# Optimization experiments

Hardware: AMD Instinct MI355X
Metric: run time of the kernel (lower is better)

## Reference

```python
import jax, jax.numpy as jnp
import numpy as np

T, Z, D_DIM = 8, 2048, 1024
N_EXP, P_SLOT, H = 64, 32, 1024
LN_EPS = 1e-5


def setup_inputs() -> dict:
    key = jax.random.key(0)
    k = jax.random.split(key, 5)
    s = 0.02
    return {
        "x": jax.random.normal(k[0], (T, Z, D_DIM), dtype=jnp.float32),
        "phi_w": jax.random.normal(k[1], (N_EXP * P_SLOT, D_DIM), dtype=jnp.float32) * s,
        "phi_b": jax.random.normal(k[2], (N_EXP * P_SLOT,), dtype=jnp.float32) * s,
        "expert_w": jax.random.normal(k[3], (N_EXP, D_DIM, H), dtype=jnp.float32) * s,
        "expert_b": jax.random.normal(k[4], (N_EXP, H), dtype=jnp.float32) * s,
    }


def reference(x, phi_w, phi_b, expert_w, expert_b):
    t, z, d = x.shape
    n = expert_w.shape[0]
    p = phi_w.shape[0] // n
    # routing logits: [t, z, n, p]
    logits = (jnp.einsum('tzd,ed->tze', x, phi_w) + phi_b).reshape(t, z, n, p)
    D = jax.nn.softmax(logits, axis=3)  # dispatch: softmax over slots p
    C = jax.nn.softmax(logits, axis=2)  # combine:  softmax over experts n
    # slot inputs, summed over batch AND tokens (as in the source einsum)
    X_tilde = jnp.einsum('tznp,tzd->npd', D, x)
    X_tilde = jnp.clip(X_tilde, -33000.0, 65000.0)
    # layer norm over last dim, no affine
    mu = jnp.mean(X_tilde, axis=-1, keepdims=True)
    var = jnp.mean(jnp.square(X_tilde - mu), axis=-1, keepdims=True)
    X_tilde = (X_tilde - mu) * jax.lax.rsqrt(var + LN_EPS)
    X_tilde = jnp.tanh(X_tilde)
    # per-expert Linear, batched over experts: [n,p,d] x [n,d,H] -> [n,p,H]
    Y_tilde = jnp.einsum('npd,ndH->npH', X_tilde, expert_w) + expert_b[:, None, :]
    # combine back to tokens: [t,z,H]
    Y = jnp.einsum('tznp,npH->tzH', C, Y_tilde)
    return Y
```

## Files before the change

### kernel.cpp

```cpp
#include <hip/hip_runtime.h>
#include <hip/hip_bf16.h>
#include <math.h>

#define TOKENS   16384
#define DDIM     1024
#define NEXP     64
#define PSLOT    32
#define NSLOTS   2048
#define HDIM     1024
#define LN_EPS   1e-5f
#define KSPLIT   8

typedef __bf16 b16x8 __attribute__((ext_vector_type(8)));
typedef float  f32x4 __attribute__((ext_vector_type(4)));

__device__ __forceinline__ unsigned short f2b(float f) {
    union { float f; unsigned u; } v; v.f = f;
    unsigned r = v.u + 0x7FFF + ((v.u >> 16) & 1);
    return (unsigned short)(r >> 16);
}
__device__ __forceinline__ float b2f(unsigned short u) {
    union { unsigned u; float f; } v; v.u = ((unsigned)u) << 16; return v.f;
}

__device__ __forceinline__ void load_lds16(const void* g, void* l) {
    __builtin_amdgcn_global_load_lds(
        (const __attribute__((address_space(1))) void*)g,
        (__attribute__((address_space(3))) void*)l, 16, 0, 0);
}

template<bool BIAS, typename OT>
__global__ __launch_bounds__(512, 2) void gemm_nt_256(
    const unsigned short* __restrict__ A,
    const unsigned short* __restrict__ B,
    const float* __restrict__ bias,
    OT* __restrict__ C,
    int M, int N, int K)
{
    __shared__ unsigned short lds[2][2][256 * 64];
    const int tid  = threadIdx.x;
    const int wave = tid >> 6;
    const int lane = tid & 63;
    const int wr = wave >> 2;
    const int wc = wave & 3;
    const int fr = lane & 15;
    const int fs = lane >> 4;
    const int kswz = ((lane & 7) ^ (lane >> 3)) * 8;

    const int gx  = (int)gridDim.x, gy = (int)gridDim.y;
    const int nwg = gx * gy;
    const int wg  = (int)blockIdx.y * gx + (int)blockIdx.x;
    const int swz = (wg & 7) * (nwg >> 3) + (wg >> 3);
    const int m0 = (swz / gx) * 256;
    const int n0 = (swz % gx) * 256;

    const int kc = K / gridDim.z;
    const int kb = blockIdx.z * kc;
    C += (size_t)blockIdx.z * M * N;
    const int NT = kc >> 6;

    f32x4 acc[8][4] = {};
    b16x8 Ag[4][2], Bf[2][2], Bs2[2][2];

#define KOF(T)   (kb + (T) * 64)

#define STAGE_A(BUF, T, R0) { \
    const int k0_ = KOF(T); \
    _Pragma("unroll") for (int hh = 0; hh < 2; ++hh) { \
        const int rp_ = (R0) + hh * 64 + wave * 8 + (lane >> 3); \
        const int L_  = ((rp_ >> 6) & 1) * 128 + ((rp_ >> 7) & 1) * 64 + (rp_ & 63); \
        load_lds16(A + (size_t)(m0 + L_) * K + k0_ + kswz, \
                   &lds[BUF][0][((R0) + hh * 64 + wave * 8) * 64]); } }

#define STAGE_B(BUF, T, R0) { \
    const int k0_ = KOF(T); \
    _Pragma("unroll") for (int hh = 0; hh < 2; ++hh) { \
        const int rp_ = (R0) + hh * 64 + wave * 8 + (lane >> 3); \
        const int L_  = ((rp_ >> 5) & 3) * 64 + ((rp_ >> 7) & 1) * 32 + (rp_ & 31); \
        load_lds16(B + (size_t)(n0 + L_) * K + k0_ + kswz, \
                   &lds[BUF][1][((R0) + hh * 64 + wave * 8) * 64]); } }

#define LDA_G(BUF, IBASE) \
    _Pragma("unroll") for (int ii = 0; ii < 4; ++ii) { \
        const int rp_ = (IBASE) + 64 * wr + ii * 16 + fr; \
        _Pragma("unroll") for (int h = 0; h < 2; ++h) \
            Ag[ii][h] = *(const b16x8*)&lds[BUF][0][rp_ * 64 + (((h * 4 + fs) ^ (rp_ & 7)) * 8)]; }

#define LDB_G(BUF, JBASE, DST) \
    _Pragma("unroll") for (int jj = 0; jj < 2; ++jj) { \
        const int rp_ = (JBASE) + 32 * wc + jj * 16 + fr; \
        _Pragma("unroll") for (int h = 0; h < 2; ++h) \
            DST[jj][h] = *(const b16x8*)&lds[BUF][1][rp_ * 64 + (((h * 4 + fs) ^ (rp_ & 7)) * 8)]; }

#define MFMA_Q(IB, JB, BREG) \
    __builtin_amdgcn_s_setprio(1); \
    _Pragma("unroll") for (int ii = 0; ii < 4; ++ii) \
    _Pragma("unroll") for (int jj = 0; jj < 2; ++jj) \
    _Pragma("unroll") for (int h = 0; h < 2; ++h) \
        acc[(IB) + ii][(JB) + jj] = __builtin_amdgcn_mfma_f32_16x16x32_bf16( \
            Ag[ii][h], BREG[jj][h], acc[(IB) + ii][(JB) + jj], 0, 0, 0); \
    __builtin_amdgcn_s_setprio(0);

#define BAR1  { __builtin_amdgcn_s_barrier(); __builtin_amdgcn_sched_barrier(0); }
#define BAR2  { __builtin_amdgcn_s_barrier(); }
#define VMW6  { asm volatile("s_waitcnt vmcnt(6)" ::: "memory"); \
                __builtin_amdgcn_sched_barrier(0); }
#define VMW0  { asm volatile("s_waitcnt vmcnt(0)" ::: "memory"); \
                __builtin_amdgcn_sched_barrier(0); }

    STAGE_A(0, 0, 0);   STAGE_B(0, 0, 0);   STAGE_B(0, 0, 128);  STAGE_A(0, 0, 128);
    STAGE_A(1, 1, 0);   STAGE_B(1, 1, 0);   STAGE_B(1, 1, 128);
    VMW6; BAR2;

    const int nit = NT >> 1;
    for (int it = 0; it < nit - 1; ++it) {
        const int t1 = 2 * it + 1;
        LDA_G(0, 0); LDB_G(0, 0, Bf);
        STAGE_A(1, t1, 128);
        BAR1; MFMA_Q(0, 0, Bf); BAR2;
        LDB_G(0, 128, Bs2);
        STAGE_A(0, t1 + 1, 0);
        BAR1; MFMA_Q(0, 2, Bs2); BAR2;
        LDA_G(0, 128);
        STAGE_B(0, t1 + 1, 0);
        BAR1; MFMA_Q(4, 2, Bs2); BAR2;
        STAGE_B(0, t1 + 1, 128);
        BAR1; MFMA_Q(4, 0, Bf); VMW6; BAR2;
        LDA_G(1, 0); LDB_G(1, 0, Bf);
        STAGE_A(0, t1 + 1, 128);
        BAR1; MFMA_Q(0, 0, Bf); BAR2;
        LDB_G(1, 128, Bs2);
        STAGE_A(1, t1 + 2, 0);
        BAR1; MFMA_Q(0, 2, Bs2); BAR2;
        LDA_G(1, 128);
        STAGE_B(1, t1 + 2, 0);
        BAR1; MFMA_Q(4, 2, Bs2); BAR2;
        STAGE_B(1, t1 + 2, 128);
        BAR1; MFMA_Q(4, 0, Bf); VMW6; BAR2;
    }

    {
        const int t1 = NT - 1;
        LDA_G(0, 0); LDB_G(0, 0, Bf);
        STAGE_A(1, t1, 128);
        BAR1; MFMA_Q(0, 0, Bf); BAR2;
        LDB_G(0, 128, Bs2);
        BAR1; MFMA_Q(0, 2, Bs2); BAR2;
        LDA_G(0, 128);
        BAR1; MFMA_Q(4, 2, Bs2); BAR2;
        BAR1; MFMA_Q(4, 0, Bf); VMW0; BAR2;
        LDA_G(1, 0); LDB_G(1, 0, Bf);
        BAR1; MFMA_Q(0, 0, Bf); BAR2;
        LDB_G(1, 128, Bs2);
        BAR1; MFMA_Q(0, 2, Bs2); BAR2;
        LDA_G(1, 128);
        BAR1; MFMA_Q(4, 2, Bs2); BAR2;
        BAR1; MFMA_Q(4, 0, Bf); BAR2;
    }

    const int col  = lane & 15;
    const int row4 = (lane >> 4) * 4;
#pragma unroll
    for (int j = 0; j < 4; ++j) {
        const int n = n0 + wc * 64 + j * 16 + col;
        const float bj = BIAS ? bias[n] : 0.f;
#pragma unroll
        for (int i = 0; i < 8; ++i) {
#pragma unroll
            for (int r = 0; r < 4; ++r) {
                const int m = m0 + wr * 128 + i * 16 + row4 + r;
                const float v = acc[i][j][r] + bj;
                if constexpr (sizeof(OT) == 2) C[(size_t)m * N + n] = f2b(v);
                else                            C[(size_t)m * N + n] = v;
            }
        }
    }
#undef KOF
#undef STAGE_A
#undef STAGE_B
#undef LDA_G
#undef LDB_G
#undef MFMA_Q
#undef BAR1
#undef BAR2
#undef VMW6
#undef VMW0
}

__global__ __launch_bounds__(256) void prep_x(
    const float* __restrict__ in, unsigned short* __restrict__ xb,
    unsigned short* __restrict__ xT)
{
    __shared__ unsigned short tile[64][68];
    const int t  = threadIdx.x;
    const int c0 = blockIdx.x * 64;
    const int r0 = blockIdx.y * 64;
    const int tr = t >> 4, tc4 = (t & 15) * 4;
#pragma unroll
    for (int i = 0; i < 4; ++i) {
        const int r = tr + i * 16;
        const float4 v = *(const float4*)&in[(size_t)(r0 + r) * DDIM + c0 + tc4];
        ushort4 o;
        o.x = f2b(v.x); o.y = f2b(v.y); o.z = f2b(v.z); o.w = f2b(v.w);
        *(ushort4*)&xb[(size_t)(r0 + r) * DDIM + c0 + tc4] = o;
        tile[tc4 + 0][r] = o.x; tile[tc4 + 1][r] = o.y;
        tile[tc4 + 2][r] = o.z; tile[tc4 + 3][r] = o.w;
    }
    __syncthreads();
#pragma unroll
    for (int i = 0; i < 4; ++i) {
        const int r = tr + i * 16;
        ushort4 o;
        o.x = tile[r][tc4 + 0]; o.y = tile[r][tc4 + 1];
        o.z = tile[r][tc4 + 2]; o.w = tile[r][tc4 + 3];
        *(ushort4*)&xT[(size_t)(c0 + r) * TOKENS + r0 + tc4] = o;
    }
}

__global__ __launch_bounds__(256) void cast_f32_bf16(
    const float* __restrict__ in, unsigned short* __restrict__ out)
{
    const size_t i = (size_t)(blockIdx.x * 256 + threadIdx.x) * 8;
    const float4 a = *(const float4*)&in[i];
    const float4 b = *(const float4*)&in[i + 4];
    ushort4 o0, o1;
    o0.x = f2b(a.x); o0.y = f2b(a.y); o0.z = f2b(a.z); o0.w = f2b(a.w);
    o1.x = f2b(b.x); o1.y = f2b(b.y); o1.z = f2b(b.z); o1.w = f2b(b.w);
    *(ushort4*)&out[i]     = o0;
    *(ushort4*)&out[i + 4] = o1;
}

__global__ __launch_bounds__(256) void softmax_both(
    const unsigned short* __restrict__ logits,
    unsigned short* __restrict__ DbT, unsigned short* __restrict__ Cb)
{
    __shared__ float ls[8][32][33];
    __shared__ float Mv[32][33], Sv[32][33];
    const int tid  = threadIdx.x;
    const int tok0 = blockIdx.x * 32;
    const int tok  = tid & 31;

    {
        const int tk = tid >> 3, pp = (tid & 7) * 4;
#pragma unroll
        for (int q = 0; q < 4; ++q) { Mv[tk][pp + q] = -1e30f; Sv[tk][pp + q] = 0.f; }
    }
    __syncthreads();

    for (int c = 0; c < 8; ++c) {
#pragma unroll
        for (int i = 0; i < 4; ++i) {
            const int flat = i * 256 + tid;
            const int row  = flat >> 5;
            const int c8   = (flat & 31) * 8;
            const unsigned short* p = &logits[(size_t)(tok0 + row) * NSLOTS + c * 256 + c8];
            const ushort4 u0 = *(const ushort4*)&p[0];
            const ushort4 u1 = *(const ushort4*)&p[4];
            float* b = &ls[c8 >> 5][row][c8 & 31];
            b[0] = b2f(u0.x); b[1] = b2f(u0.y); b[2] = b2f(u0.z); b[3] = b2f(u0.w);
            b[4] = b2f(u1.x); b[5] = b2f(u1.y); b[6] = b2f(u1.z); b[7] = b2f(u1.w);
        }
        __syncthreads();

        {
            const int nl = tid >> 5;
            const float* r = ls[nl][tok];
            float m = r[0];
#pragma unroll
            for (int p = 1; p < PSLOT; ++p) m = fmaxf(m, r[p]);
            float s = 0.f;
#pragma unroll
            for (int p = 0; p < PSLOT; ++p) s += __expf(r[p] - m);
            const float inv = 1.f / s;
            unsigned short* o = &DbT[(size_t)(c * 256 + nl * 32) * TOKENS + tok0 + tok];
#pragma unroll
            for (int p = 0; p < PSLOT; ++p)
                o[(size_t)p * TOKENS] = f2b(__expf(r[p] - m) * inv);
        }

        {
            const int pg = tid >> 5;
#pragma unroll
            for (int k = 0; k < 4; ++k) {
                const int p = pg * 4 + k;
                float m8 = ls[0][tok][p];
#pragma unroll
                for (int n = 1; n < 8; ++n) m8 = fmaxf(m8, ls[n][tok][p]);
                float s8 = 0.f;
#pragma unroll
                for (int n = 0; n < 8; ++n) s8 += __expf(ls[n][tok][p] - m8);
                const float M = Mv[tok][p], S = Sv[tok][p];
                const float Mn = fmaxf(M, m8);
                Sv[tok][p] = S * __expf(M - Mn) + s8 * __expf(m8 - Mn);
                Mv[tok][p] = Mn;
            }
        }
        __syncthreads();
    }

    {
        const int tk = tid >> 3, pp = (tid & 7) * 4;
#pragma unroll
        for (int q = 0; q < 4; ++q) Sv[tk][pp + q] = 1.f / Sv[tk][pp + q];
    }
    __syncthreads();

    for (int c = 0; c < 8; ++c) {
#pragma unroll
        for (int i = 0; i < 4; ++i) {
            const int flat = i * 256 + tid;
            const int row  = flat >> 5;
            const int c8   = (flat & 31) * 8;
            const int p    = c8 & 31;
            const unsigned short* q = &logits[(size_t)(tok0 + row) * NSLOTS + c * 256 + c8];
            const ushort4 u0 = *(const ushort4*)&q[0];
            const ushort4 u1 = *(const ushort4*)&q[4];
            ushort4 o0, o1;
            o0.x = f2b(__expf(b2f(u0.x) - Mv[row][p + 0]) * Sv[row][p + 0]);
            o0.y = f2b(__expf(b2f(u0.y) - Mv[row][p + 1]) * Sv[row][p + 1]);
            o0.z = f2b(__expf(b2f(u0.z) - Mv[row][p + 2]) * Sv[row][p + 2]);
            o0.w = f2b(__expf(b2f(u0.w) - Mv[row][p + 3]) * Sv[row][p + 3]);
            o1.x = f2b(__expf(b2f(u1.x) - Mv[row][p + 4]) * Sv[row][p + 4]);
            o1.y = f2b(__expf(b2f(u1.y) - Mv[row][p + 5]) * Sv[row][p + 5]);
            o1.z = f2b(__expf(b2f(u1.z) - Mv[row][p + 6]) * Sv[row][p + 6]);
            o1.w = f2b(__expf(b2f(u1.w) - Mv[row][p + 7]) * Sv[row][p + 7]);
            unsigned short* d = &Cb[(size_t)(tok0 + row) * NSLOTS + c * 256 + c8];
            *(ushort4*)&d[0] = o0;
            *(ushort4*)&d[4] = o1;
        }
    }
}

__global__ __launch_bounds__(256) void reduce_ln_tanh(
    const float* __restrict__ parts, float* __restrict__ Xt)
{
    const int tid = threadIdx.x;
    const size_t off = (size_t)blockIdx.x * DDIM + tid * 4;
    __shared__ float red1[4], red2[4];

    float4 v = *(const float4*)&parts[off];
#pragma unroll
    for (int s = 1; s < KSPLIT; ++s) {
        const float4 p = *(const float4*)&parts[(size_t)s * NSLOTS * DDIM + off];
        v.x += p.x; v.y += p.y; v.z += p.z; v.w += p.w;
    }
    v.x = fminf(fmaxf(v.x, -33000.f), 65000.f);
    v.y = fminf(fmaxf(v.y, -33000.f), 65000.f);
    v.z = fminf(fmaxf(v.z, -33000.f), 65000.f);
    v.w = fminf(fmaxf(v.w, -33000.f), 65000.f);

    float s = v.x + v.y + v.z + v.w;
#pragma unroll
    for (int off2 = 32; off2 > 0; off2 >>= 1) s += __shfl_down(s, off2);
    if ((tid & 63) == 0) red1[tid >> 6] = s;
    __syncthreads();
    const float mu = (red1[0] + red1[1] + red1[2] + red1[3]) * (1.f / DDIM);

    const float dx = v.x - mu, dy = v.y - mu, dz = v.z - mu, dw = v.w - mu;
    float q = dx * dx + dy * dy + dz * dz + dw * dw;
#pragma unroll
    for (int off2 = 32; off2 > 0; off2 >>= 1) q += __shfl_down(q, off2);
    if ((tid & 63) == 0) red2[tid >> 6] = q;
    __syncthreads();
    const float var = (red2[0] + red2[1] + red2[2] + red2[3]) * (1.f / DDIM);
    const float sc = rsqrtf(var + LN_EPS);

    float4 o;
    o.x = tanhf(dx * sc); o.y = tanhf(dy * sc);
    o.z = tanhf(dz * sc); o.w = tanhf(dw * sc);
    *(float4*)&Xt[off] = o;
}

__global__ __launch_bounds__(256) void expert_gemm(
    const float* __restrict__ Xt, const float* __restrict__ W,
    const float* __restrict__ bias, unsigned short* __restrict__ YtT)
{
    const int n   = blockIdx.y;
    const int h0  = blockIdx.x * 128;
    const int tid = threadIdx.x;
    __shared__ float As[2][32][32];
    __shared__ float Bs[2][32][128];
    __shared__ unsigned short ty[128][36];

    const int r  = tid >> 4;
    const int c8 = (tid & 15) * 8;
    float acc0[8], acc1[8];
#pragma unroll
    for (int j = 0; j < 8; ++j) { acc0[j] = 0.f; acc1[j] = 0.f; }

    const float* Wn = W + (size_t)n * DDIM * HDIM;
    const float* Xn = Xt + (size_t)n * 32 * DDIM;

#define EG_STAGE(T, BUF) { \
    const int k0_ = (T) * 32; \
    _Pragma("unroll") for (int i = 0; i < 4; ++i) { \
        const int flat = i * 256 + tid; \
        const int brow = flat >> 5, bch = (flat & 31) * 4; \
        load_lds16(Wn + (size_t)(k0_ + brow) * HDIM + h0 + bch, \
                   &Bs[BUF][brow][bch]); } \
    { const int arow = tid >> 3, ach = (tid & 7) * 4; \
      load_lds16(Xn + (size_t)arow * DDIM + k0_ + ach, &As[BUF][arow][ach]); } }

    EG_STAGE(0, 0);
    for (int t = 0; t < 32; ++t) {
        const int buf = t & 1;
        if (t < 31) {
            EG_STAGE(t + 1, (t + 1) & 1);
            asm volatile("s_waitcnt vmcnt(5)" ::: "memory");
        } else {
            asm volatile("s_waitcnt vmcnt(0)" ::: "memory");
        }
        __builtin_amdgcn_sched_barrier(0);
        __builtin_amdgcn_s_barrier();
#pragma unroll
        for (int kk = 0; kk < 32; ++kk) {
            const float a0 = As[buf][r][kk];
            const float a1 = As[buf][r + 16][kk];
            const float4 b0 = *(const float4*)&Bs[buf][kk][c8];
            const float4 b1 = *(const float4*)&Bs[buf][kk][c8 + 4];
            acc0[0] = fmaf(a0, b0.x, acc0[0]); acc0[1] = fmaf(a0, b0.y, acc0[1]);
            acc0[2] = fmaf(a0, b0.z, acc0[2]); acc0[3] = fmaf(a0, b0.w, acc0[3]);
            acc0[4] = fmaf(a0, b1.x, acc0[4]); acc0[5] = fmaf(a0, b1.y, acc0[5]);
            acc0[6] = fmaf(a0, b1.z, acc0[6]); acc0[7] = fmaf(a0, b1.w, acc0[7]);
            acc1[0] = fmaf(a1, b0.x, acc1[0]); acc1[1] = fmaf(a1, b0.y, acc1[1]);
            acc1[2] = fmaf(a1, b0.z, acc1[2]); acc1[3] = fmaf(a1, b0.w, acc1[3]);
            acc1[4] = fmaf(a1, b1.x, acc1[4]); acc1[5] = fmaf(a1, b1.y, acc1[5]);
            acc1[6] = fmaf(a1, b1.z, acc1[6]); acc1[7] = fmaf(a1, b1.w, acc1[7]);
        }
        __builtin_amdgcn_s_barrier();
    }
#undef EG_STAGE

    const float* bn = bias + (size_t)n * HDIM + h0;
#pragma unroll
    for (int j = 0; j < 8; ++j) {
        const float bj = bn[c8 + j];
        ty[c8 + j][r]      = f2b(acc0[j] + bj);
        ty[c8 + j][r + 16] = f2b(acc1[j] + bj);
    }
    __syncthreads();

    const int row = tid >> 1, q = (tid & 1) * 16;
    unsigned short* dst = &YtT[(size_t)(h0 + row) * NSLOTS + n * 32 + q];
#pragma unroll
    for (int u = 0; u < 4; ++u)
        *(ushort4*)&dst[u * 4] = *(const ushort4*)&ty[row][q + u * 4];
}

extern "C" void kernel_launch(void* const* d_in, const int* in_sizes, int n_in,
                              void* d_out, int out_size, void* d_ws, size_t ws_size,
                              hipStream_t stream)
{
    const float* x        = (const float*)d_in[0];
    const float* phi_w    = (const float*)d_in[1];
    const float* phi_b    = (const float*)d_in[2];
    const float* expert_w = (const float*)d_in[3];
    const float* expert_b = (const float*)d_in[4];
    float* out = (float*)d_out;

    char* ws = (char*)d_ws;
    const size_t MB = 1u << 20;
    unsigned short* xb     = (unsigned short*)(ws);
    unsigned short* xT     = (unsigned short*)(ws +  32 * MB);
    unsigned short* pwb    = (unsigned short*)(ws +  64 * MB);
    unsigned short* logbf  = (unsigned short*)(ws +  68 * MB);
    unsigned short* DbT    = (unsigned short*)(ws + 132 * MB);
    unsigned short* Cb     = (unsigned short*)(ws + 196 * MB);
    float*          parts  = (float*)(ws + 260 * MB);
    float*          Xt     = (float*)(ws + 324 * MB);
    unsigned short* YtT    = (unsigned short*)(ws + 332 * MB);

    prep_x<<<dim3(DDIM / 64, TOKENS / 64), 256, 0, stream>>>(x, xb, xT);
    cast_f32_bf16<<<NSLOTS * DDIM / (256 * 8), 256, 0, stream>>>(phi_w, pwb);

    gemm_nt_256<true, unsigned short>
        <<<dim3(NSLOTS / 256, TOKENS / 256), 512, 0, stream>>>(
            xb, pwb, phi_b, logbf, TOKENS, NSLOTS, DDIM);

    softmax_both<<<TOKENS / 32, 256, 0, stream>>>(logbf, DbT, Cb);

    gemm_nt_256<false, float>
        <<<dim3(DDIM / 256, NSLOTS / 256, KSPLIT), 512, 0, stream>>>(
            DbT, xT, nullptr, parts, NSLOTS, DDIM, TOKENS);

    reduce_ln_tanh<<<NSLOTS, 256, 0, stream>>>(parts, Xt);

    expert_gemm<<<dim3(HDIM / 128, NEXP), 256, 0, stream>>>(
        Xt, expert_w, expert_b, YtT);

    gemm_nt_256<false, float>
        <<<dim3(HDIM / 256, TOKENS / 256), 512, 0, stream>>>(
            Cb, YtT, nullptr, out, TOKENS, HDIM, NSLOTS);
}
```

Measured before the change: 733.7 us.

## Store split-K partials in bf16 and widen expert GEMM tiles

The split-K slot-input GEMM now writes its partial sums as bf16 instead of fp32, which halves the partial-buffer traffic for both the writer and the reduce/LayerNorm kernel that sums them. The expert GEMM is retiled from 256 threads and 128 columns to 512 threads and 256 columns per block. The A tile is now loaded with 4-byte LDS loads and the wait count is adjusted to match. Rounding partials to bf16 before the reduction adds error ahead of the LayerNorm, and the expert GEMM now runs with half as many blocks.

```diff
diff --git a/kernel.cpp b/kernel.cpp
--- a/kernel.cpp
+++ b/kernel.cpp
@@ -27,6 +27,11 @@
     __builtin_amdgcn_global_load_lds(
         (const __attribute__((address_space(1))) void*)g,
         (__attribute__((address_space(3))) void*)l, 16, 0, 0);
+}
+__device__ __forceinline__ void load_lds4(const void* g, void* l) {
+    __builtin_amdgcn_global_load_lds(
+        (const __attribute__((address_space(1))) void*)g,
+        (__attribute__((address_space(3))) void*)l, 4, 0, 0);
 }
 
 template<bool BIAS, typename OT>
@@ -332,17 +337,17 @@
 }
 
 __global__ __launch_bounds__(256) void reduce_ln_tanh(
-    const float* __restrict__ parts, float* __restrict__ Xt)
+    const unsigned short* __restrict__ parts, float* __restrict__ Xt)
 {
     const int tid = threadIdx.x;
     const size_t off = (size_t)blockIdx.x * DDIM + tid * 4;
     __shared__ float red1[4], red2[4];
 
-    float4 v = *(const float4*)&parts[off];
-#pragma unroll
-    for (int s = 1; s < KSPLIT; ++s) {
-        const float4 p = *(const float4*)&parts[(size_t)s * NSLOTS * DDIM + off];
-        v.x += p.x; v.y += p.y; v.z += p.z; v.w += p.w;
+    float4 v = {0.f, 0.f, 0.f, 0.f};
+#pragma unroll
+    for (int s = 0; s < KSPLIT; ++s) {
+        const ushort4 p = *(const ushort4*)&parts[(size_t)s * NSLOTS * DDIM + off];
+        v.x += b2f(p.x); v.y += b2f(p.y); v.z += b2f(p.z); v.w += b2f(p.w);
     }
     v.x = fminf(fmaxf(v.x, -33000.f), 65000.f);
     v.y = fminf(fmaxf(v.y, -33000.f), 65000.f);
@@ -371,19 +376,19 @@
     *(float4*)&Xt[off] = o;
 }
 
-__global__ __launch_bounds__(256) void expert_gemm(
+__global__ __launch_bounds__(512, 2) void expert_gemm(
     const float* __restrict__ Xt, const float* __restrict__ W,
     const float* __restrict__ bias, unsigned short* __restrict__ YtT)
 {
     const int n   = blockIdx.y;
-    const int h0  = blockIdx.x * 128;
+    const int h0  = blockIdx.x * 256;
     const int tid = threadIdx.x;
     __shared__ float As[2][32][32];
-    __shared__ float Bs[2][32][128];
-    __shared__ unsigned short ty[128][36];
-
-    const int r  = tid >> 4;
-    const int c8 = (tid & 15) * 8;
+    __shared__ float Bs[2][32][256];
+    __shared__ unsigned short ty[256][36];
+
+    const int r2 = tid >> 5;
+    const int c8 = (tid & 31) * 8;
     float acc0[8], acc1[8];
 #pragma unroll
     for (int j = 0; j < 8; ++j) { acc0[j] = 0.f; acc1[j] = 0.f; }
@@ -394,19 +399,21 @@
 #define EG_STAGE(T, BUF) { \
     const int k0_ = (T) * 32; \
     _Pragma("unroll") for (int i = 0; i < 4; ++i) { \
-        const int flat = i * 256 + tid; \
-        const int brow = flat >> 5, bch = (flat & 31) * 4; \
-        load_lds16(Wn + (size_t)(k0_ + brow) * HDIM + h0 + bch, \
-                   &Bs[BUF][brow][bch]); } \
-    { const int arow = tid >> 3, ach = (tid & 7) * 4; \
-      load_lds16(Xn + (size_t)arow * DDIM + k0_ + ach, &As[BUF][arow][ach]); } }
+        const int flat = i * 512 + tid; \
+        const int brow = flat >> 6, bc4 = (flat & 63) * 4; \
+        load_lds16(Wn + (size_t)(k0_ + brow) * HDIM + h0 + bc4, \
+                   &Bs[BUF][brow][bc4]); } \
+    _Pragma("unroll") for (int i = 0; i < 2; ++i) { \
+        const int flat = i * 512 + tid; \
+        const int arow = flat >> 5, ac = flat & 31; \
+        load_lds4(Xn + (size_t)arow * DDIM + k0_ + ac, &As[BUF][arow][ac]); } }
 
     EG_STAGE(0, 0);
     for (int t = 0; t < 32; ++t) {
         const int buf = t & 1;
         if (t < 31) {
             EG_STAGE(t + 1, (t + 1) & 1);
-            asm volatile("s_waitcnt vmcnt(5)" ::: "memory");
+            asm volatile("s_waitcnt vmcnt(6)" ::: "memory");
         } else {
             asm volatile("s_waitcnt vmcnt(0)" ::: "memory");
         }
@@ -414,8 +421,8 @@
         __builtin_amdgcn_s_barrier();
 #pragma unroll
         for (int kk = 0; kk < 32; ++kk) {
-            const float a0 = As[buf][r][kk];
-            const float a1 = As[buf][r + 16][kk];
+            const float a0 = As[buf][r2][kk];
+            const float a1 = As[buf][r2 + 16][kk];
             const float4 b0 = *(const float4*)&Bs[buf][kk][c8];
             const float4 b1 = *(const float4*)&Bs[buf][kk][c8 + 4];
             acc0[0] = fmaf(a0, b0.x, acc0[0]); acc0[1] = fmaf(a0, b0.y, acc0[1]);
@@ -435,8 +442,8 @@
 #pragma unroll
     for (int j = 0; j < 8; ++j) {
         const float bj = bn[c8 + j];
-        ty[c8 + j][r]      = f2b(acc0[j] + bj);
-        ty[c8 + j][r + 16] = f2b(acc1[j] + bj);
+        ty[c8 + j][r2]      = f2b(acc0[j] + bj);
+        ty[c8 + j][r2 + 16] = f2b(acc1[j] + bj);
     }
     __syncthreads();
 
@@ -466,9 +473,9 @@
     unsigned short* logbf  = (unsigned short*)(ws +  68 * MB);
     unsigned short* DbT    = (unsigned short*)(ws + 132 * MB);
     unsigned short* Cb     = (unsigned short*)(ws + 196 * MB);
-    float*          parts  = (float*)(ws + 260 * MB);
-    float*          Xt     = (float*)(ws + 324 * MB);
-    unsigned short* YtT    = (unsigned short*)(ws + 332 * MB);
+    unsigned short* parts  = (unsigned short*)(ws + 260 * MB);
+    float*          Xt     = (float*)(ws + 292 * MB);
+    unsigned short* YtT    = (unsigned short*)(ws + 300 * MB);
 
     prep_x<<<dim3(DDIM / 64, TOKENS / 64), 256, 0, stream>>>(x, xb, xT);
     cast_f32_bf16<<<NSLOTS * DDIM / (256 * 8), 256, 0, stream>>>(phi_w, pwb);
@@ -479,13 +486,13 @@
 
     softmax_both<<<TOKENS / 32, 256, 0, stream>>>(logbf, DbT, Cb);
 
-    gemm_nt_256<false, float>
+    gemm_nt_256<false, unsigned short>
         <<<dim3(DDIM / 256, NSLOTS / 256, KSPLIT), 512, 0, stream>>>(
             DbT, xT, nullptr, parts, NSLOTS, DDIM, TOKENS);
 
     reduce_ln_tanh<<<NSLOTS, 256, 0, stream>>>(parts, Xt);
 
-    expert_gemm<<<dim3(HDIM / 128, NEXP), 256, 0, stream>>>(
+    expert_gemm<<<dim3(HDIM / 256, NEXP), 512, 0, stream>>>(
         Xt, expert_w, expert_b, YtT);
 
     gemm_nt_256<false, float>
```

New measurement: 745.5 us. About the same (+1.6%).
